# Kernel optimization log

Hardware: AMD Instinct MI355X
Metric: run time of the kernel (lower is better)

Reference implementation:

```python
import jax, jax.numpy as jnp
import numpy as np


def _normalize(x):
    # channel mean-subtract then channel L2 normalize, as in MIDMs.forward
    x = x - x.mean(axis=1, keepdims=True)
    return x / jnp.linalg.norm(x, axis=1, keepdims=True)


def setup_inputs() -> dict:
    key = jax.random.key(0)
    ks = jax.random.split(key, 6)
    B, C, H, W = 2, 256, 64, 64
    return {
        "trg_out": jax.random.normal(ks[0], (B, C, H, W), jnp.float32),
        "src_out": jax.random.normal(ks[1], (B, C, H, W), jnp.float32),
        "ref_out": jax.random.normal(ks[2], (B, C, H, W), jnp.float32),
        "src_feats": jax.random.normal(ks[3], (B, 4, H, W), jnp.float32),
        "ref_feats": jax.random.normal(ks[4], (B, 4, H, W), jnp.float32),
        "ref_semantics": jax.random.uniform(ks[5], (B, 151, H, W), jnp.float32),
    }


def reference(trg_out, src_out, ref_out, src_feats, ref_feats, ref_semantics):
    B, C, H, W = trg_out.shape
    L = H * W
    # normalized matching features, flattened over spatial positions
    t = _normalize(trg_out).reshape(B, C, L)   # [B, C, Lt]
    s = _normalize(src_out).reshape(B, C, L)   # [B, C, Ls]
    r = _normalize(ref_out).reshape(B, C, L)

    # Correlation.correlation: dense cosine affinity between all position pairs
    corr_src = jnp.einsum("bci,bcj->bij", t, s)  # [B, Lt, Ls]
    corr_ref = jnp.einsum("bci,bcj->bij", t, r)

    # soft_warp: softmax over source positions, attention-weighted gather
    attn_src = jax.nn.softmax(corr_src, axis=-1)
    attn_ref = jax.nn.softmax(corr_ref, axis=-1)

    warped_src_feat = jnp.einsum("bij,bcj->bci", attn_src,
                                 src_feats.reshape(B, -1, L)).reshape(B, -1, H, W)
    warped_ref_feat = jnp.einsum("bij,bcj->bci", attn_ref,
                                 ref_feats.reshape(B, -1, L)).reshape(B, -1, H, W)
    warped_ref_seg = jnp.einsum("bij,bcj->bci", attn_ref,
                                ref_semantics.reshape(B, -1, L)).reshape(B, -1, H, W)
    return warped_src_feat, warped_ref_feat, warped_ref_seg
```

## Files before the change

### kernel.cpp

```cpp
#include <hip/hip_runtime.h>
#include <hip/hip_bf16.h>
#include <cstdint>
#include <cstddef>

typedef unsigned short u16;
typedef __attribute__((ext_vector_type(8))) __bf16 bf16x8;
typedef __attribute__((ext_vector_type(4))) unsigned u32x4;
typedef __attribute__((ext_vector_type(16))) float f32x16;

#define LPOS 4096
#define CDIM 256
#define LDSBUF 13312

#if __has_builtin(__builtin_amdgcn_exp2f)
#define EXP2(x) __builtin_amdgcn_exp2f(x)
#else
#define EXP2(x) exp2f(x)
#endif

#define GLOAD_LDS16(g, l)                                                      \
  __builtin_amdgcn_global_load_lds(                                            \
      (const __attribute__((address_space(1))) void*)(g),                      \
      (__attribute__((address_space(3))) void*)(l), 16, 0, 0)

__device__ __forceinline__ unsigned f2bfbits(float x) {
  union { float f; unsigned u; } v; v.f = x;
  return (v.u + 0x7FFFu + ((v.u >> 16) & 1u)) >> 16;
}
__device__ __forceinline__ unsigned packbf(float a, float b) {
  __hip_bfloat162 h2 = __float22bfloat162_rn(make_float2(a, b));
  return *(unsigned*)&h2;
}

__global__ void norm_fused(const float* __restrict__ t_in,
                           const float* __restrict__ s_in,
                           const float* __restrict__ r_in,
                           u16* __restrict__ qn, u16* __restrict__ ksn,
                           u16* __restrict__ krn) {
  __shared__ float tile[256 * 33];
  __shared__ float sums[256], sqs[256];
  __shared__ float mv[32], ivv[32];
  int idx = blockIdx.x;
  int ab = idx >> 7, lt = idx & 127;
  int arr = ab >> 1, b = ab & 1;
  int l0 = lt * 32;
  const float* inp = (arr == 0 ? t_in : arr == 1 ? s_in : r_in) + (size_t)b * CDIM * LPOS;
  u16* outp = (arr == 0 ? qn : arr == 1 ? ksn : krn) + (size_t)b * LPOS * CDIM;
  float scale = (arr == 0) ? 1.4426950408889634f : 1.0f;
  int t = threadIdx.x;
  int cg = t >> 5, l = t & 31;
  float sum = 0.f, sq = 0.f;
#pragma unroll 8
  for (int cc = 0; cc < 32; ++cc) {
    int c = cg * 32 + cc;
    float v = inp[(size_t)c * LPOS + l0 + l];
    tile[c * 33 + l] = v;
    sum += v; sq += v * v;
  }
  sums[t] = sum; sqs[t] = sq;
  __syncthreads();
  if (t < 32) {
    float s = 0.f, q = 0.f;
#pragma unroll
    for (int g = 0; g < 8; ++g) { s += sums[g * 32 + t]; q += sqs[g * 32 + t]; }
    float mean = s * (1.0f / CDIM);
    float nsq = q - s * s * (1.0f / CDIM);
    mv[t] = mean;
    ivv[t] = rsqrtf(fmaxf(nsq, 1e-20f)) * scale;
  }
  __syncthreads();
  int c2 = t & 127, ph = t >> 7;
#pragma unroll 4
  for (int rr = 0; rr < 16; ++rr) {
    int pos = ph + rr * 2;
    float m = mv[pos], iv = ivv[pos];
    float v0 = (tile[(2 * c2) * 33 + pos] - m) * iv;
    float v1 = (tile[(2 * c2 + 1) * 33 + pos] - m) * iv;
    *(unsigned*)&outp[(size_t)(l0 + pos) * CDIM + 2 * c2] = packbf(v0, v1);
  }
}

__global__ void build_v(const float* __restrict__ sf, const float* __restrict__ rf,
                        const float* __restrict__ sem,
                        u16* __restrict__ vs, u16* __restrict__ vr) {
  int t = blockIdx.x * 256 + threadIdx.x;
  const int NVS = 2 * 32 * 4096;
  if (t < NVS) {
    int b = t >> 17;
    int c = (t >> 12) & 31;
    int j = t & 4095;
    float v = (c < 4) ? sf[((size_t)b * 4 + c) * LPOS + j] : (c == 4 ? 1.0f : 0.0f);
    vs[t] = (u16)f2bfbits(v);
  } else {
    int t2 = t - NVS;
    if (t2 < 2 * 160 * 4096) {
      int b = t2 / (160 * 4096);
      int rr = t2 % (160 * 4096);
      int c = rr >> 12, j = rr & 4095;
      float v = (c < 151) ? sem[((size_t)b * 151 + c) * LPOS + j]
              : (c < 155) ? rf[((size_t)b * 4 + (c - 151)) * LPOS + j]
              : (c == 155) ? 1.0f : 0.0f;
      vr[((size_t)b * 160 + c) * LPOS + j] = (u16)f2bfbits(v);
    }
  }
}

template <int CT>
__device__ __forceinline__ void flash_body(
    const u16* __restrict__ qb, const u16* __restrict__ kb,
    const u16* __restrict__ vb, float* __restrict__ dst,
    u16 (*lds)[LDSBUF], int wave, int lane, int i_wave, int j_base, int iters) {
  int h = lane >> 5, ln = lane & 31;

  bf16x8 qf[16];
  const u16* qrow = qb + (size_t)(i_wave + ln) * CDIM;
#pragma unroll
  for (int kt = 0; kt < 16; ++kt)
    qf[kt] = *(const bf16x8*)(qrow + kt * 16 + h * 8);
#pragma unroll
  for (int kt = 0; kt < 16; ++kt)
    asm volatile("" : "+v"(*(u32x4*)&qf[kt]));

  f32x16 O[CT];
#pragma unroll
  for (int c = 0; c < CT; ++c)
#pragma unroll
    for (int t = 0; t < 16; ++t) O[c][t] = 0.0f;

  auto stage = [&](int j0s, int buf) {
#pragma unroll
    for (int g = 0; g < 4; ++g) {
      int G = wave * 4 + g;
      int j = 2 * G + h;
      GLOAD_LDS16(kb + (size_t)(j0s + j) * CDIM + (ln ^ (j & 7)) * 8,
                  &lds[buf][G * 512]);
    }
    if constexpr (CT == 5) {
#pragma unroll
      for (int g = 0; g < 3; ++g) {
        int s = wave * 3 + g;
        if (s < 10) {
          int f = s * 64 + lane;
          int p = f / 160;
          int c = f - p * 160;
          GLOAD_LDS16(vb + (size_t)c * LPOS + j0s + p * 8,
                      &lds[buf][8192 + s * 512]);
        }
      }
    }
  };

  int kread_base = ln * 256 + 8 * (h ^ (ln & 1));
  int q = (ln >> 1) & 3;
  const u16* ka[4];
#pragma unroll
  for (int m = 0; m < 4; ++m) ka[m] = &lds[0][kread_base + 16 * (m ^ q)];
  const u16* va = &lds[0][8192 + h * 1280 + ln * 8];

  auto iter_body = [&](int jt, int buf) {
    int j0 = j_base + jt * 32;
    int bo = buf * LDSBUF;
    __syncthreads();

    bf16x8 vf[2];
    if constexpr (CT == 1) {
#pragma unroll
      for (int kt2 = 0; kt2 < 2; ++kt2)
        vf[kt2] = *(const bf16x8*)(vb + (size_t)ln * LPOS + j0 + (2 * kt2 + h) * 8);
    }
    if (jt + 1 < iters) stage(j0 + 32, buf ^ 1);
    f32x16 Sa, Sb;
#pragma unroll
    for (int t = 0; t < 16; ++t) { Sa[t] = 0.0f; Sb[t] = 0.0f; }
#pragma unroll
    for (int kt = 0; kt < 16; kt += 2) {
      bf16x8 ka0 = *(const bf16x8*)(ka[kt & 3] + 64 * (kt >> 2) + bo);
      Sa = __builtin_amdgcn_mfma_f32_32x32x16_bf16(ka0, qf[kt], Sa, 0, 0, 0);
      bf16x8 ka1 = *(const bf16x8*)(ka[(kt + 1) & 3] + 64 * ((kt + 1) >> 2) + bo);
      Sb = __builtin_amdgcn_mfma_f32_32x32x16_bf16(ka1, qf[kt + 1], Sb, 0, 0, 0);
    }
    f32x16 S;
#pragma unroll
    for (int t = 0; t < 16; ++t) S[t] = EXP2(Sa[t] + Sb[t]);

    bf16x8 pb[2];
#pragma unroll
    for (int kh = 0; kh < 2; ++kh) {
      unsigned c0 = packbf(S[kh * 8 + 0], S[kh * 8 + 1]);
      unsigned c1 = packbf(S[kh * 8 + 2], S[kh * 8 + 3]);
      unsigned c2 = packbf(S[kh * 8 + 4], S[kh * 8 + 5]);
      unsigned c3 = packbf(S[kh * 8 + 6], S[kh * 8 + 7]);
      unsigned keep0 = h ? c2 : c0, keep1 = h ? c3 : c1;
      unsigned send0 = h ? c0 : c2, send1 = h ? c1 : c3;
      unsigned recv0 = (unsigned)__shfl_xor((int)send0, 32, 64);
      unsigned recv1 = (unsigned)__shfl_xor((int)send1, 32, 64);
      union { unsigned u[4]; bf16x8 v; } tmp;
      tmp.u[0] = h ? recv0 : keep0;
      tmp.u[1] = h ? recv1 : keep1;
      tmp.u[2] = h ? keep0 : recv0;
      tmp.u[3] = h ? keep1 : recv1;
      pb[kh] = tmp.v;
    }

#pragma unroll
    for (int ct = 0; ct < CT; ++ct)
#pragma unroll
      for (int kt2 = 0; kt2 < 2; ++kt2) {
        bf16x8 vax;
        if constexpr (CT == 5)
          vax = *(const bf16x8*)(va + kt2 * 2560 + ct * 256 + bo);
        else
          vax = vf[kt2];
        O[ct] = __builtin_amdgcn_mfma_f32_32x32x16_bf16(vax, pb[kt2], O[ct], 0, 0, 0);
      }
  };

  stage(j_base, 0);
  for (int jt = 0; jt < iters; jt += 2) {
    iter_body(jt, 0);
    iter_body(jt + 1, 1);
  }

#pragma unroll
  for (int ct = 0; ct < CT; ++ct)
#pragma unroll
    for (int t = 0; t < 16; ++t) {
      int c = ct * 32 + (t & 3) + 8 * (t >> 2) + 4 * h;
      dst[(size_t)c * LPOS + i_wave + ln] = O[ct][t];
    }
}

__global__ __launch_bounds__(256, 2) void flash(
    const u16* __restrict__ qn, const u16* __restrict__ ksn, const u16* __restrict__ krn,
    const u16* __restrict__ vs, const u16* __restrict__ vr,
    float* __restrict__ nsrc, float* __restrict__ nref,
    int nch_src, int nch_ref) {
  __shared__ u16 lds[2][LDSBUF];
  int tid = threadIdx.x;
  int wave = tid >> 6, lane = tid & 63;
  int idx = blockIdx.x;
  int third = idx / 3, m = idx - third * 3;
  if (m == 0) {
    int r = third;
    int chunk = r >> 6, b = (r >> 5) & 1, wgi = r & 31;
    int jchunk = LPOS / nch_ref;
    flash_body<5>(qn + (size_t)b * LPOS * CDIM, krn + (size_t)b * LPOS * CDIM,
                  vr + (size_t)b * 160 * LPOS,
                  nref + (size_t)(chunk * 2 + b) * 160 * LPOS,
                  lds, wave, lane, wgi * 128 + wave * 32, chunk * jchunk,
                  jchunk / 32);
  } else {
    int r = idx - third - 1;
    int chunk = r >> 6, b = (r >> 5) & 1, wgi = r & 31;
    int jchunk = LPOS / nch_src;
    flash_body<1>(qn + (size_t)b * LPOS * CDIM, ksn + (size_t)b * LPOS * CDIM,
                  vs + (size_t)b * 32 * LPOS,
                  nsrc + (size_t)(chunk * 2 + b) * 32 * LPOS,
                  lds, wave, lane, wgi * 128 + wave * 32, chunk * jchunk,
                  jchunk / 32);
  }
}

__global__ void finalize(const float* __restrict__ nsrc, const float* __restrict__ nref,
                         float* __restrict__ out, int nch_src, int nch_ref) {
  int t = blockIdx.x * 256 + threadIdx.x;
  if (t >= 1302528) return;
  if (t < 32768) {
    int b = t >> 14, c = (t >> 12) & 3, i = t & 4095;
    float num = 0.f, den = 0.f;
    for (int k = 0; k < nch_src; ++k) {
      const float* base = nsrc + ((size_t)(k * 2 + b) * 32) * LPOS;
      num += base[(size_t)c * LPOS + i];
      den += base[(size_t)4 * LPOS + i];
    }
    out[t] = num / den;
  } else if (t < 65536) {
    int t1 = t - 32768;
    int b = t1 >> 14, c = (t1 >> 12) & 3, i = t1 & 4095;
    float num = 0.f, den = 0.f;
    for (int k = 0; k < nch_ref; ++k) {
      const float* base = nref + ((size_t)(k * 2 + b) * 160) * LPOS;
      num += base[(size_t)(151 + c) * LPOS + i];
      den += base[(size_t)155 * LPOS + i];
    }
    out[t] = num / den;
  } else {
    int t2 = t - 65536;
    int b = t2 / 618496;
    int rr = t2 % 618496;
    int c = rr >> 12, i = rr & 4095;
    float num = 0.f, den = 0.f;
    for (int k = 0; k < nch_ref; ++k) {
      const float* base = nref + ((size_t)(k * 2 + b) * 160) * LPOS;
      num += base[(size_t)c * LPOS + i];
      den += base[(size_t)155 * LPOS + i];
    }
    out[t] = num / den;
  }
}

extern "C" void kernel_launch(void* const* d_in, const int* in_sizes, int n_in,
                              void* d_out, int out_size, void* d_ws, size_t ws_size,
                              hipStream_t stream) {
  const float* trg  = (const float*)d_in[0];
  const float* srcp = (const float*)d_in[1];
  const float* refp = (const float*)d_in[2];
  const float* sfeat = (const float*)d_in[3];
  const float* rfeat = (const float*)d_in[4];
  const float* rsem  = (const float*)d_in[5];
  float* out = (float*)d_out;

  char* ws = (char*)d_ws;
  size_t o = 0;
  auto alloc = [&](size_t bytes) -> char* {
    char* p = ws + o;
    o += (bytes + 255) & ~(size_t)255;
    return p;
  };
  u16* qn  = (u16*)alloc(2ull * LPOS * CDIM * 2);
  u16* ksn = (u16*)alloc(2ull * LPOS * CDIM * 2);
  u16* krn = (u16*)alloc(2ull * LPOS * CDIM * 2);
  u16* vs  = (u16*)alloc(2ull * 32 * LPOS * 2);
  u16* vr  = (u16*)alloc(2ull * 160 * LPOS * 2);

  size_t fixed = o;
  int nch_ref = 8;
  for (;;) {
    size_t need = fixed + 512 +
                  (size_t)(2 * nch_ref) * 2 * 32 * LPOS * 4 +
                  (size_t)nch_ref * 2 * 160 * LPOS * 4;
    if (need <= ws_size || nch_ref == 1) break;
    nch_ref >>= 1;
  }
  int nch_src = 2 * nch_ref;
  float* nsrc = (float*)alloc((size_t)nch_src * 2 * 32 * LPOS * 4);
  float* nref = (float*)alloc((size_t)nch_ref * 2 * 160 * LPOS * 4);

  hipLaunchKernelGGL(norm_fused, dim3(768), dim3(256), 0, stream,
                     trg, srcp, refp, qn, ksn, krn);
  hipLaunchKernelGGL(build_v, dim3(6144), dim3(256), 0, stream,
                     sfeat, rfeat, rsem, vs, vr);
  hipLaunchKernelGGL(flash, dim3(64 * nch_ref * 3), dim3(256), 0, stream,
                     qn, ksn, krn, vs, vr, nsrc, nref, nch_src, nch_ref);
  hipLaunchKernelGGL(finalize, dim3(5088), dim3(256), 0, stream,
                     nsrc, nref, out, nch_src, nch_ref);
}
```

Measured before the change: 168.3 us.

## Triple-buffer flash K/V staging with explicit vmcnt waits and vectorize finalize

The flash kernel moves from double-buffered to triple-buffered LDS staging. It prefetches two tiles ahead and uses explicit s_waitcnt vmcnt plus a raw s_barrier in place of __syncthreads, so global-to-LDS loads overlap more with MFMA work. It also rebalances V staging across waves, skips writing the unused padded output channels, and makes finalize process four elements per thread with float4 loads and stores. The LDS footprint grows by half, which may limit occupancy at two blocks per CU, and the hand-tuned vmcnt counts must match the exact number of loads issued per stage.

Measured after the change: 169.5 us. About the same (+0.7%).

```diff
diff --git a/kernel.cpp b/kernel.cpp
--- a/kernel.cpp
+++ b/kernel.cpp
@@ -138,7 +138,7 @@
     if constexpr (CT == 5) {
 #pragma unroll
       for (int g = 0; g < 3; ++g) {
-        int s = wave * 3 + g;
+        int s = wave + g * 4;
         if (s < 10) {
           int f = s * 64 + lane;
           int p = f / 160;
@@ -157,10 +157,24 @@
   for (int m = 0; m < 4; ++m) ka[m] = &lds[0][kread_base + 16 * (m ^ q)];
   const u16* va = &lds[0][8192 + h * 1280 + ln * 8];
 
-  auto iter_body = [&](int jt, int buf) {
+  stage(j_base, 0);
+  if (iters > 1) stage(j_base + 32, 1);
+
+  int buf = 0;
+  for (int jt = 0; jt < iters; ++jt) {
     int j0 = j_base + jt * 32;
     int bo = buf * LDSBUF;
-    __syncthreads();
+
+    if (jt == iters - 1) {
+      asm volatile("s_waitcnt vmcnt(0)" ::: "memory");
+    } else if (CT == 5) {
+      asm volatile("s_waitcnt vmcnt(6)" ::: "memory");
+    } else {
+      asm volatile("s_waitcnt vmcnt(4)" ::: "memory");
+    }
+    __builtin_amdgcn_sched_barrier(0);
+    __builtin_amdgcn_s_barrier();
+    __builtin_amdgcn_sched_barrier(0);
 
     bf16x8 vf[2];
     if constexpr (CT == 1) {
@@ -168,7 +182,11 @@
       for (int kt2 = 0; kt2 < 2; ++kt2)
         vf[kt2] = *(const bf16x8*)(vb + (size_t)ln * LPOS + j0 + (2 * kt2 + h) * 8);
     }
-    if (jt + 1 < iters) stage(j0 + 32, buf ^ 1);
+    if (jt + 2 < iters) {
+      int b2 = buf ? buf - 1 : 2;
+      stage(j0 + 64, b2);
+    }
+
     f32x16 Sa, Sb;
 #pragma unroll
     for (int t = 0; t < 16; ++t) { Sa[t] = 0.0f; Sb[t] = 0.0f; }
@@ -213,20 +231,18 @@
           vax = vf[kt2];
         O[ct] = __builtin_amdgcn_mfma_f32_32x32x16_bf16(vax, pb[kt2], O[ct], 0, 0, 0);
       }
-  };
-
-  stage(j_base, 0);
-  for (int jt = 0; jt < iters; jt += 2) {
-    iter_body(jt, 0);
-    iter_body(jt + 1, 1);
-  }
-
+
+    buf = (buf == 2) ? 0 : buf + 1;
+  }
+
+  const int climit = (CT == 1) ? 5 : 156;
 #pragma unroll
   for (int ct = 0; ct < CT; ++ct)
 #pragma unroll
     for (int t = 0; t < 16; ++t) {
       int c = ct * 32 + (t & 3) + 8 * (t >> 2) + 4 * h;
-      dst[(size_t)c * LPOS + i_wave + ln] = O[ct][t];
+      if (c < climit)
+        dst[(size_t)c * LPOS + i_wave + ln] = O[ct][t];
     }
 }
 
@@ -235,7 +251,7 @@
     const u16* __restrict__ vs, const u16* __restrict__ vr,
     float* __restrict__ nsrc, float* __restrict__ nref,
     int nch_src, int nch_ref) {
-  __shared__ u16 lds[2][LDSBUF];
+  __shared__ u16 lds[3][LDSBUF];
   int tid = threadIdx.x;
   int wave = tid >> 6, lane = tid & 63;
   int idx = blockIdx.x;
@@ -263,40 +279,45 @@
 
 __global__ void finalize(const float* __restrict__ nsrc, const float* __restrict__ nref,
                          float* __restrict__ out, int nch_src, int nch_ref) {
-  int t = blockIdx.x * 256 + threadIdx.x;
-  if (t >= 1302528) return;
-  if (t < 32768) {
-    int b = t >> 14, c = (t >> 12) & 3, i = t & 4095;
-    float num = 0.f, den = 0.f;
+  int v = blockIdx.x * 256 + threadIdx.x;
+  if (v >= 325632) return;
+  float nx = 0.f, ny = 0.f, nz = 0.f, nw = 0.f;
+  float dx = 0.f, dy = 0.f, dz = 0.f, dw = 0.f;
+  if (v < 8192) {
+    int b = v >> 12, c = (v >> 10) & 3, i4 = v & 1023;
     for (int k = 0; k < nch_src; ++k) {
       const float* base = nsrc + ((size_t)(k * 2 + b) * 32) * LPOS;
-      num += base[(size_t)c * LPOS + i];
-      den += base[(size_t)4 * LPOS + i];
-    }
-    out[t] = num / den;
-  } else if (t < 65536) {
-    int t1 = t - 32768;
-    int b = t1 >> 14, c = (t1 >> 12) & 3, i = t1 & 4095;
-    float num = 0.f, den = 0.f;
+      float4 n4 = ((const float4*)(base + (size_t)c * LPOS))[i4];
+      float4 d4 = ((const float4*)(base + (size_t)4 * LPOS))[i4];
+      nx += n4.x; ny += n4.y; nz += n4.z; nw += n4.w;
+      dx += d4.x; dy += d4.y; dz += d4.z; dw += d4.w;
+    }
+  } else if (v < 16384) {
+    int v1 = v - 8192;
+    int b = v1 >> 12, c = (v1 >> 10) & 3, i4 = v1 & 1023;
     for (int k = 0; k < nch_ref; ++k) {
       const float* base = nref + ((size_t)(k * 2 + b) * 160) * LPOS;
-      num += base[(size_t)(151 + c) * LPOS + i];
-      den += base[(size_t)155 * LPOS + i];
-    }
-    out[t] = num / den;
+      float4 n4 = ((const float4*)(base + (size_t)(151 + c) * LPOS))[i4];
+      float4 d4 = ((const float4*)(base + (size_t)155 * LPOS))[i4];
+      nx += n4.x; ny += n4.y; nz += n4.z; nw += n4.w;
+      dx += d4.x; dy += d4.y; dz += d4.z; dw += d4.w;
+    }
   } else {
-    int t2 = t - 65536;
-    int b = t2 / 618496;
-    int rr = t2 % 618496;
-    int c = rr >> 12, i = rr & 4095;
-    float num = 0.f, den = 0.f;
+    int v2 = v - 16384;
+    int b = v2 / 154624;
+    int rr = v2 - b * 154624;
+    int c = rr >> 10, i4 = rr & 1023;
     for (int k = 0; k < nch_ref; ++k) {
       const float* base = nref + ((size_t)(k * 2 + b) * 160) * LPOS;
-      num += base[(size_t)c * LPOS + i];
-      den += base[(size_t)155 * LPOS + i];
-    }
-    out[t] = num / den;
-  }
+      float4 n4 = ((const float4*)(base + (size_t)c * LPOS))[i4];
+      float4 d4 = ((const float4*)(base + (size_t)155 * LPOS))[i4];
+      nx += n4.x; ny += n4.y; nz += n4.z; nw += n4.w;
+      dx += d4.x; dy += d4.y; dz += d4.z; dw += d4.w;
+    }
+  }
+  float4 r;
+  r.x = nx / dx; r.y = ny / dy; r.z = nz / dz; r.w = nw / dw;
+  ((float4*)out)[v] = r;
 }
 
 extern "C" void kernel_launch(void* const* d_in, const int* in_sizes, int n_in,
@@ -342,6 +363,6 @@
                      sfeat, rfeat, rsem, vs, vr);
   hipLaunchKernelGGL(flash, dim3(64 * nch_ref * 3), dim3(256), 0, stream,
                      qn, ksn, krn, vs, vr, nsrc, nref, nch_src, nch_ref);
-  hipLaunchKernelGGL(finalize, dim3(5088), dim3(256), 0, stream,
+  hipLaunchKernelGGL(finalize, dim3(1272), dim3(256), 0, stream,
                      nsrc, nref, out, nch_src, nch_ref);
 }
```
